# Performance work log

Hardware: AMD Instinct MI355X
Metric: run time of the kernel (lower is better)

## Reference

```python
import jax, jax.numpy as jnp
import numpy as np

HEADS = 16
DIM_HEAD = 64
SCALE = DIM_HEAD ** -0.5


def setup_inputs() -> dict:
    key = jax.random.key(0)
    k1, k2, k3, k4 = jax.random.split(key, 4)
    b, n, dim = 2, 2048, 1024
    inner = HEADS * DIM_HEAD  # 1024
    x = jax.random.normal(k1, (b, n, dim), dtype=jnp.float32)
    # binary keep-mask (multiplicative, as in the original module)
    seq_mask = (jax.random.uniform(k2, (b, n)) < 0.9).astype(jnp.float32)
    # weights stored [in, out] (transpose of torch Linear layout)
    w_qkv = jax.random.normal(k3, (dim, inner * 3), dtype=jnp.float32) * (dim ** -0.5)
    w_out = jax.random.normal(k4, (inner, dim), dtype=jnp.float32) * (inner ** -0.5)
    return {"x": x, "seq_mask": seq_mask, "w_qkv": w_qkv, "w_out": w_out}


def reference(x, seq_mask, w_qkv, w_out):
    b, n, dim = x.shape
    qkv = x @ w_qkv                                   # [b, n, 3*inner]
    q, k, v = jnp.split(qkv, 3, axis=-1)
    split_heads = lambda t: t.reshape(b, n, HEADS, DIM_HEAD).transpose(0, 2, 1, 3)
    q, k, v = split_heads(q), split_heads(k), split_heads(v)  # [b, h, n, d]
    dots = jnp.einsum('bhid,bhjd->bhij', q, k) * SCALE        # [b, h, n, n]
    # multiplicative mask, broadcast over heads and query index i; mask depends on key index j
    dots = dots * seq_mask[:, None, None, :]
    attn = jax.nn.softmax(dots, axis=-1)
    out = jnp.einsum('bhij,bhjd->bhid', attn, v)              # [b, h, n, d]
    out = out.transpose(0, 2, 1, 3).reshape(b, n, HEADS * DIM_HEAD)
    return out @ w_out                                        # dropout p=0 -> identity
```

## Files before the change

### kernel.cpp

```cpp
#include <hip/hip_runtime.h>
#include <hip/hip_bf16.h>

using bf16 = __hip_bfloat16;
typedef __attribute__((ext_vector_type(8))) short short8;
typedef __attribute__((ext_vector_type(4))) float floatx4;
typedef __attribute__((ext_vector_type(16))) float floatx16;
typedef __attribute__((ext_vector_type(4))) int int4v;

#define MFMA_BF16(a, b, c) __builtin_amdgcn_mfma_f32_16x16x32_bf16((a), (b), (c), 0, 0, 0)
#define MFMA32(a, b, c) __builtin_amdgcn_mfma_f32_32x32x16_bf16((a), (b), (c), 0, 0, 0)

#if defined(__has_builtin)
#if __has_builtin(__builtin_amdgcn_permlane32_swap)
#define HAS_PLSWAP 1
#endif
#endif

__device__ __forceinline__ void gload_lds16(const bf16* g, bf16* l) {
  __builtin_amdgcn_global_load_lds((__attribute__((address_space(1))) void*)g,
                                   (__attribute__((address_space(3))) void*)l,
                                   16, 0, 0);
}

__device__ __forceinline__ unsigned short bfbits(float f) {
  bf16 b = __float2bfloat16(f);
  return *reinterpret_cast<unsigned short*>(&b);
}

__device__ __forceinline__ unsigned pk2(float a, float b) {
  return (unsigned)bfbits(a) | ((unsigned)bfbits(b) << 16);
}

__device__ __forceinline__ int swz32(int r) { return (r & 7) ^ ((r >> 3) & 3); }

#define KSCALE 0.18033688011112042f

__global__ __launch_bounds__(256)
void probemask_k(const void* __restrict__ msrc, bf16* __restrict__ dst,
                 int* __restrict__ flag) {
  __shared__ int any;
  const int tid = threadIdx.x;
  if (tid == 0) any = 0;
  __syncthreads();
  const unsigned* mw = (const unsigned*)msrc;
  int bad = 0;
#pragma unroll
  for (int i = 0; i < 4; i++) {
    unsigned w = mw[tid * 4 + i];
    if (w != 0u && w != 0x3F800000u) bad = 1;
  }
  if (bad) atomicOr(&any, 1);
  __syncthreads();
  const int isbf = any;
  if (tid == 0) flag[0] = isbf;
  if (isbf) {
#pragma unroll
    for (int i = 0; i < 2; i++)
      ((int4*)dst)[tid * 2 + i] = ((const int4*)msrc)[tid * 2 + i];
  } else {
#pragma unroll
    for (int i = 0; i < 4; i++) {
      float4 v = ((const float4*)msrc)[tid * 4 + i];
      int o = tid * 16 + i * 4;
      dst[o + 0] = __float2bfloat16(v.x);
      dst[o + 1] = __float2bfloat16(v.y);
      dst[o + 2] = __float2bfloat16(v.z);
      dst[o + 3] = __float2bfloat16(v.w);
    }
  }
}

__global__ __launch_bounds__(256)
void cvt_k(const void* __restrict__ src, bf16* __restrict__ dst, int n,
           const int* __restrict__ flag) {
  if (*flag) return;
  int i = (blockIdx.x * 256 + threadIdx.x) * 4;
  if (i >= n) return;
  float4 v = ((const float4*)src)[i >> 2];
  dst[i + 0] = __float2bfloat16(v.x);
  dst[i + 1] = __float2bfloat16(v.y);
  dst[i + 2] = __float2bfloat16(v.z);
  dst[i + 3] = __float2bfloat16(v.w);
}

__global__ __launch_bounds__(256)
void transpose2_k(const void* __restrict__ in0, bf16* __restrict__ out0,
                  const void* __restrict__ in1, bf16* __restrict__ out1,
                  const int* __restrict__ flag) {
  __shared__ bf16 tile[32][33];
  const int isbf = *flag;
  constexpr int R = 1024;
  const void* in;
  bf16* out;
  int C, bx;
  if (blockIdx.x < 96) { in = in0; out = out0; C = 3072; bx = blockIdx.x * 32; }
  else                 { in = in1; out = out1; C = 1024; bx = (blockIdx.x - 96) * 32; }
  int by = blockIdx.y * 32;
  int tx = threadIdx.x & 31, ty = threadIdx.x >> 5;
#pragma unroll
  for (int i = 0; i < 4; i++) {
    size_t idx = (size_t)(by + ty + i * 8) * C + bx + tx;
    tile[ty + i * 8][tx] =
        isbf ? ((const bf16*)in)[idx] : __float2bfloat16(((const float*)in)[idx]);
  }
  __syncthreads();
#pragma unroll
  for (int i = 0; i < 4; i++)
    out[(size_t)(bx + ty + i * 8) * R + by + tx] = tile[tx][ty + i * 8];
}

template <int MODE>
__global__ __launch_bounds__(256, 2)
void gemm_k(const bf16* __restrict__ A, const bf16* __restrict__ Aalt,
            const bf16* __restrict__ Bt,
            bf16* __restrict__ Qo, bf16* __restrict__ Ko, bf16* __restrict__ Vo,
            void* __restrict__ Co, const bf16* __restrict__ Mk,
            const int* __restrict__ flag) {
  constexpr int K = 1024;
  __shared__ __align__(16) bf16 As[128 * 32];
  __shared__ __align__(16) bf16 Bs[128 * 32];

  const int tid = threadIdx.x;
  const int lane = tid & 63;
  const int wv = tid >> 6;
  const int wm = wv & 1, wn = wv >> 1;
  const int l15 = lane & 15, quad = lane >> 4;

  const int bm = blockIdx.y * 128;
  const int bn = blockIdx.x * 128;

  const int sml = tid >> 2;
  const int sg = (tid & 3) ^ ((sml >> 1) & 3);

  const int isbf = *flag;
  const bf16* Ab = (MODE == 0 && isbf) ? Aalt : A;

  floatx4 acc[4][4] = {};

  for (int k0 = 0; k0 < K; k0 += 32) {
    __syncthreads();
    const bf16* a0 = Ab + (size_t)(bm + sml) * K + k0 + sg * 8;
    gload_lds16(a0, &As[tid * 8]);
    gload_lds16(a0 + (size_t)64 * K, &As[2048 + tid * 8]);
    const bf16* b0 = Bt + (size_t)(bn + sml) * K + k0 + sg * 8;
    gload_lds16(b0, &Bs[tid * 8]);
    gload_lds16(b0 + (size_t)64 * K, &Bs[2048 + tid * 8]);
    __syncthreads();

    short8 af[4], bfr[4];
#pragma unroll
    for (int mi = 0; mi < 4; mi++) {
      int m = wm * 64 + mi * 16 + l15;
      af[mi] = *(const short8*)&As[m * 32 + ((quad ^ ((m >> 1) & 3)) * 8)];
    }
#pragma unroll
    for (int ni = 0; ni < 4; ni++) {
      int n = wn * 64 + ni * 16 + l15;
      bfr[ni] = *(const short8*)&Bs[n * 32 + ((quad ^ ((n >> 1) & 3)) * 8)];
    }
#pragma unroll
    for (int mi = 0; mi < 4; mi++)
#pragma unroll
      for (int ni = 0; ni < 4; ni++)
        acc[mi][ni] = MFMA_BF16(af[mi], bfr[ni], acc[mi][ni]);
  }

#pragma unroll
  for (int mi = 0; mi < 4; mi++) {
    const int row0 = bm + wm * 64 + mi * 16 + quad * 4;
#pragma unroll
    for (int ni = 0; ni < 4; ni++) {
      const int col = bn + wn * 64 + ni * 16 + l15;
      if (MODE == 0) {
        const int sec = col >> 10;
        const int cc = col & 1023;
        const int h = cc >> 6, d = cc & 63;
        const int b_idx = row0 >> 11;
        const int nn0 = row0 & 2047;
        if (sec == 0) {
          bf16* dst = Qo + (size_t)(b_idx * 16 + h) * 131072 + (size_t)nn0 * 64 + d;
#pragma unroll
          for (int r = 0; r < 4; r++) dst[r * 64] = __float2bfloat16(acc[mi][ni][r]);
        } else if (sec == 1) {
          const bf16* mrow = Mk + (size_t)b_idx * 2048 + nn0;
          bf16* dst = Ko + (size_t)(b_idx * 16 + h) * 131072 + (size_t)nn0 * 64 + d;
#pragma unroll
          for (int r = 0; r < 4; r++)
            dst[r * 64] = __float2bfloat16(acc[mi][ni][r] * KSCALE *
                                           __bfloat162float(mrow[r]));
        } else {
          bf16* dst = Vo + (size_t)(b_idx * 16 + h) * 131072 + (size_t)d * 2048 + nn0;
#pragma unroll
          for (int r = 0; r < 4; r++) dst[r] = __float2bfloat16(acc[mi][ni][r]);
        }
      } else {
        if (isbf) {
          bf16* C2 = (bf16*)Co;
#pragma unroll
          for (int r = 0; r < 4; r++)
            C2[(size_t)(row0 + r) * 1024 + col] = __float2bfloat16(acc[mi][ni][r]);
        } else {
          float* C2 = (float*)Co;
#pragma unroll
          for (int r = 0; r < 4; r++)
            C2[(size_t)(row0 + r) * 1024 + col] = acc[mi][ni][r];
        }
      }
    }
  }
}

__global__ __launch_bounds__(256, 4)
void flash_k(const bf16* __restrict__ Q, const bf16* __restrict__ K,
             const bf16* __restrict__ VT, bf16* __restrict__ AO) {
  __shared__ __align__(16) bf16 Ks[2][4096];
  __shared__ __align__(16) bf16 Vs[2][4096];
#ifndef HAS_PLSWAP
  __shared__ __align__(16) bf16 Ps[8192];
#endif

  const int tid = threadIdx.x;
  const int lane = tid & 63;
  const int w = tid >> 6;
  const int l31 = lane & 31;
  const int l5h = lane >> 5;
  const int sw = swz32(l31);

  const int qt = blockIdx.x & 15;
  const int hl = blockIdx.x >> 4;
  const int b_idx = hl >> 4, h = hl & 15;

  const bf16* Qh = Q + (size_t)hl * 131072;
  const bf16* Kh = K + (size_t)hl * 131072;
  const bf16* Vh = VT + (size_t)hl * 131072;

  const int qbase = qt * 128 + w * 32;
  const int qrow = qbase + l31;

  short8 qf[4];
#pragma unroll
  for (int c = 0; c < 4; c++)
    qf[c] = *(const short8*)&Qh[(size_t)qrow * 64 + c * 16 + l5h * 8];

  floatx16 o_acc[2] = {};
  float rsum = 0.f;

#ifndef HAS_PLSWAP
  bf16* Psw = Ps + w * 2048;
#endif

  const int sjj = tid >> 3;
  const int sgp = (tid & 7) ^ swz32(sjj);

  gload_lds16(&Kh[(size_t)sjj * 64 + sgp * 8], &Ks[0][tid * 8]);
  gload_lds16(&Kh[(size_t)(32 + sjj) * 64 + sgp * 8], &Ks[0][2048 + tid * 8]);
  gload_lds16(&Vh[(size_t)sjj * 2048 + sgp * 8], &Vs[0][tid * 8]);
  gload_lds16(&Vh[(size_t)(32 + sjj) * 2048 + sgp * 8], &Vs[0][2048 + tid * 8]);

  for (int it = 0; it < 32; ++it) {
    const int b = it & 1;
    __syncthreads();
    if (it < 31) {
      const int j1 = (it + 1) * 64;
      gload_lds16(&Kh[(size_t)(j1 + sjj) * 64 + sgp * 8], &Ks[b ^ 1][tid * 8]);
      gload_lds16(&Kh[(size_t)(j1 + 32 + sjj) * 64 + sgp * 8], &Ks[b ^ 1][2048 + tid * 8]);
      gload_lds16(&Vh[(size_t)sjj * 2048 + j1 + sgp * 8], &Vs[b ^ 1][tid * 8]);
      gload_lds16(&Vh[(size_t)(32 + sjj) * 2048 + j1 + sgp * 8], &Vs[b ^ 1][2048 + tid * 8]);
    }

    floatx16 s[2] = {};
#pragma unroll
    for (int kt = 0; kt < 2; kt++) {
      const int key = kt * 32 + l31;
#pragma unroll
      for (int c = 0; c < 4; c++) {
        const int g = c * 2 + l5h;
        short8 kf = *(const short8*)&Ks[b][key * 64 + ((g ^ sw) * 8)];
        s[kt] = MFMA32(kf, qf[c], s[kt]);
      }
    }

    float rs = 0.f;
#pragma unroll
    for (int kt = 0; kt < 2; kt++)
#pragma unroll
      for (int r = 0; r < 16; r++) {
        const float p = __builtin_amdgcn_exp2f(s[kt][r]);
        s[kt][r] = p;
        rs += p;
      }
    rs += __shfl_xor(rs, 32, 64);
    rsum += rs;

    short8 pf[4];
#ifdef HAS_PLSWAP
#pragma unroll
    for (int kt = 0; kt < 2; kt++) {
      unsigned pd[4][2];
#pragma unroll
      for (int rg = 0; rg < 4; rg++) {
        pd[rg][0] = pk2(s[kt][rg * 4 + 0], s[kt][rg * 4 + 1]);
        pd[rg][1] = pk2(s[kt][rg * 4 + 2], s[kt][rg * 4 + 3]);
      }
#pragma unroll
      for (int cp = 0; cp < 2; cp++) {
        auto ra = __builtin_amdgcn_permlane32_swap(pd[cp * 2][0], pd[cp * 2 + 1][0],
                                                   false, false);
        auto rb = __builtin_amdgcn_permlane32_swap(pd[cp * 2][1], pd[cp * 2 + 1][1],
                                                   false, false);
        int4v pi;
        pi[0] = (int)ra[0];
        pi[1] = (int)rb[0];
        pi[2] = (int)ra[1];
        pi[3] = (int)rb[1];
        pf[kt * 2 + cp] = *(short8*)&pi;
      }
    }
#else
#pragma unroll
    for (int kt = 0; kt < 2; kt++)
#pragma unroll
      for (int rg = 0; rg < 4; rg++) {
        ushort4 u;
        u.x = bfbits(s[kt][rg * 4 + 0]);
        u.y = bfbits(s[kt][rg * 4 + 1]);
        u.z = bfbits(s[kt][rg * 4 + 2]);
        u.w = bfbits(s[kt][rg * 4 + 3]);
        const int g = kt * 4 + rg;
        *(ushort4*)&Psw[l31 * 64 + ((g ^ sw) * 8) + l5h * 4] = u;
      }
    __builtin_amdgcn_wave_barrier();
#pragma unroll
    for (int c = 0; c < 4; c++) {
      const int g = c * 2 + l5h;
      pf[c] = *(const short8*)&Psw[l31 * 64 + ((g ^ sw) * 8)];
    }
#endif

#pragma unroll
    for (int dt = 0; dt < 2; dt++) {
      const int d = dt * 32 + l31;
#pragma unroll
      for (int c = 0; c < 4; c++) {
        const int g = c * 2 + l5h;
        short8 vf = *(const short8*)&Vs[b][d * 64 + ((g ^ sw) * 8)];
        o_acc[dt] = MFMA32(vf, pf[c], o_acc[dt]);
      }
    }
  }

  const float rinv = 1.f / rsum;
  bf16* orow = AO + (size_t)(b_idx * 2048 + qbase + l31) * 1024 + h * 64;
#pragma unroll
  for (int dt = 0; dt < 2; dt++)
#pragma unroll
    for (int rg = 0; rg < 4; rg++) {
      ushort4 u;
      u.x = bfbits(o_acc[dt][rg * 4 + 0] * rinv);
      u.y = bfbits(o_acc[dt][rg * 4 + 1] * rinv);
      u.z = bfbits(o_acc[dt][rg * 4 + 2] * rinv);
      u.w = bfbits(o_acc[dt][rg * 4 + 3] * rinv);
      *(ushort4*)&orow[dt * 32 + rg * 8 + l5h * 4] = u;
    }
}

extern "C" void kernel_launch(void* const* d_in, const int* in_sizes, int n_in,
                              void* d_out, int out_size, void* d_ws, size_t ws_size,
                              hipStream_t stream) {
  const void* x     = d_in[0];
  const void* mask  = d_in[1];
  const void* w_qkv = d_in[2];
  const void* w_out = d_in[3];

  bf16* ws    = (bf16*)d_ws;
  bf16* xb    = ws;
  bf16* AO    = ws;
  bf16* wqkvT = ws + 4194304;
  bf16* woutT = wqkvT + 3145728;
  bf16* Qb    = woutT + 1048576;
  bf16* Kb    = Qb + 4194304;
  bf16* maskb = Kb + 4194304;
  int*  flag  = (int*)(maskb + 4096);
  bf16* VT    = (bf16*)d_out;

  probemask_k<<<1, 256, 0, stream>>>(mask, maskb, flag);
  cvt_k<<<4096, 256, 0, stream>>>(x, xb, 4194304, flag);
  transpose2_k<<<dim3(128, 32), 256, 0, stream>>>(w_qkv, wqkvT, w_out, woutT, flag);
  gemm_k<0><<<dim3(24, 32), 256, 0, stream>>>(xb, (const bf16*)x, wqkvT, Qb, Kb, VT,
                                              nullptr, maskb, flag);
  flash_k<<<512, 256, 0, stream>>>(Qb, Kb, VT, AO);
  gemm_k<1><<<dim3(8, 32), 256, 0, stream>>>(AO, nullptr, woutT, nullptr, nullptr,
                                             nullptr, d_out, nullptr, flag);
}
```

Measured before the change: 203.9 us.

## Split flash attention key range across two wave groups per block

The flash kernel now launches 512 threads per block. Two groups of four waves each process half of the key sequence for the same 128 queries, using separate double-buffered K/V LDS regions. Their partial outputs and row sums are combined through shared memory at the end. This raises the number of waves working on each query tile, with 512 blocks on a GPU of this size, at the cost of more LDS per block, an extra reduction step and fewer blocks resident per CU.

```diff
diff --git a/kernel.cpp b/kernel.cpp
--- a/kernel.cpp
+++ b/kernel.cpp
@@ -29,6 +29,20 @@
 
 __device__ __forceinline__ unsigned pk2(float a, float b) {
   return (unsigned)bfbits(a) | ((unsigned)bfbits(b) << 16);
+}
+
+__device__ __forceinline__ void plswap(unsigned A, unsigned B, int l5h,
+                                       unsigned& out0, unsigned& out1) {
+#ifdef HAS_PLSWAP
+  auto r = __builtin_amdgcn_permlane32_swap(A, B, false, false);
+  out0 = r[0];
+  out1 = r[1];
+#else
+  unsigned sa = (unsigned)__shfl_xor((int)A, 32, 64);
+  unsigned sb = (unsigned)__shfl_xor((int)B, 32, 64);
+  out0 = l5h ? sb : A;
+  out1 = l5h ? B : sa;
+#endif
 }
 
 __device__ __forceinline__ int swz32(int r) { return (r & 7) ^ ((r >> 3) & 3); }
@@ -210,18 +224,16 @@
   }
 }
 
-__global__ __launch_bounds__(256, 4)
+__global__ __launch_bounds__(512, 2)
 void flash_k(const bf16* __restrict__ Q, const bf16* __restrict__ K,
              const bf16* __restrict__ VT, bf16* __restrict__ AO) {
-  __shared__ __align__(16) bf16 Ks[2][4096];
-  __shared__ __align__(16) bf16 Vs[2][4096];
-#ifndef HAS_PLSWAP
-  __shared__ __align__(16) bf16 Ps[8192];
-#endif
+  __shared__ __align__(16) bf16 smem[32768];
 
   const int tid = threadIdx.x;
   const int lane = tid & 63;
   const int w = tid >> 6;
+  const int strm = w >> 2;
+  const int wl = w & 3;
   const int l31 = lane & 31;
   const int l5h = lane >> 5;
   const int sw = swz32(l31);
@@ -234,8 +246,12 @@
   const bf16* Kh = K + (size_t)hl * 131072;
   const bf16* Vh = VT + (size_t)hl * 131072;
 
-  const int qbase = qt * 128 + w * 32;
+  const int qbase = qt * 128 + wl * 32;
   const int qrow = qbase + l31;
+  const int koff = strm * 1024;
+
+  bf16* KsS = smem + strm * 8192;
+  bf16* VsS = smem + 16384 + strm * 8192;
 
   short8 qf[4];
 #pragma unroll
@@ -245,27 +261,28 @@
   floatx16 o_acc[2] = {};
   float rsum = 0.f;
 
-#ifndef HAS_PLSWAP
-  bf16* Psw = Ps + w * 2048;
-#endif
-
-  const int sjj = tid >> 3;
-  const int sgp = (tid & 7) ^ swz32(sjj);
-
-  gload_lds16(&Kh[(size_t)sjj * 64 + sgp * 8], &Ks[0][tid * 8]);
-  gload_lds16(&Kh[(size_t)(32 + sjj) * 64 + sgp * 8], &Ks[0][2048 + tid * 8]);
-  gload_lds16(&Vh[(size_t)sjj * 2048 + sgp * 8], &Vs[0][tid * 8]);
-  gload_lds16(&Vh[(size_t)(32 + sjj) * 2048 + sgp * 8], &Vs[0][2048 + tid * 8]);
-
-  for (int it = 0; it < 32; ++it) {
+  const int ts = tid & 255;
+  const int sjj = ts >> 3;
+  const int sgp = (ts & 7) ^ swz32(sjj);
+
+  gload_lds16(&Kh[(size_t)(koff + sjj) * 64 + sgp * 8], &KsS[ts * 8]);
+  gload_lds16(&Kh[(size_t)(koff + 32 + sjj) * 64 + sgp * 8], &KsS[2048 + ts * 8]);
+  gload_lds16(&Vh[(size_t)sjj * 2048 + koff + sgp * 8], &VsS[ts * 8]);
+  gload_lds16(&Vh[(size_t)(32 + sjj) * 2048 + koff + sgp * 8], &VsS[2048 + ts * 8]);
+
+  for (int it = 0; it < 16; ++it) {
     const int b = it & 1;
+    bf16* Ksb = KsS + b * 4096;
+    bf16* Vsb = VsS + b * 4096;
     __syncthreads();
-    if (it < 31) {
-      const int j1 = (it + 1) * 64;
-      gload_lds16(&Kh[(size_t)(j1 + sjj) * 64 + sgp * 8], &Ks[b ^ 1][tid * 8]);
-      gload_lds16(&Kh[(size_t)(j1 + 32 + sjj) * 64 + sgp * 8], &Ks[b ^ 1][2048 + tid * 8]);
-      gload_lds16(&Vh[(size_t)sjj * 2048 + j1 + sgp * 8], &Vs[b ^ 1][tid * 8]);
-      gload_lds16(&Vh[(size_t)(32 + sjj) * 2048 + j1 + sgp * 8], &Vs[b ^ 1][2048 + tid * 8]);
+    if (it < 15) {
+      const int j1 = koff + (it + 1) * 64;
+      bf16* Ksn = KsS + (b ^ 1) * 4096;
+      bf16* Vsn = VsS + (b ^ 1) * 4096;
+      gload_lds16(&Kh[(size_t)(j1 + sjj) * 64 + sgp * 8], &Ksn[ts * 8]);
+      gload_lds16(&Kh[(size_t)(j1 + 32 + sjj) * 64 + sgp * 8], &Ksn[2048 + ts * 8]);
+      gload_lds16(&Vh[(size_t)sjj * 2048 + j1 + sgp * 8], &Vsn[ts * 8]);
+      gload_lds16(&Vh[(size_t)(32 + sjj) * 2048 + j1 + sgp * 8], &Vsn[2048 + ts * 8]);
     }
 
     floatx16 s[2] = {};
@@ -275,7 +292,7 @@
 #pragma unroll
       for (int c = 0; c < 4; c++) {
         const int g = c * 2 + l5h;
-        short8 kf = *(const short8*)&Ks[b][key * 64 + ((g ^ sw) * 8)];
+        short8 kf = *(const short8*)&Ksb[key * 64 + ((g ^ sw) * 8)];
         s[kt] = MFMA32(kf, qf[c], s[kt]);
       }
     }
@@ -293,7 +310,6 @@
     rsum += rs;
 
     short8 pf[4];
-#ifdef HAS_PLSWAP
 #pragma unroll
     for (int kt = 0; kt < 2; kt++) {
       unsigned pd[4][2];
@@ -304,38 +320,17 @@
       }
 #pragma unroll
       for (int cp = 0; cp < 2; cp++) {
-        auto ra = __builtin_amdgcn_permlane32_swap(pd[cp * 2][0], pd[cp * 2 + 1][0],
-                                                   false, false);
-        auto rb = __builtin_amdgcn_permlane32_swap(pd[cp * 2][1], pd[cp * 2 + 1][1],
-                                                   false, false);
+        unsigned ra0, ra1, rb0, rb1;
+        plswap(pd[cp * 2][0], pd[cp * 2 + 1][0], l5h, ra0, ra1);
+        plswap(pd[cp * 2][1], pd[cp * 2 + 1][1], l5h, rb0, rb1);
         int4v pi;
-        pi[0] = (int)ra[0];
-        pi[1] = (int)rb[0];
-        pi[2] = (int)ra[1];
-        pi[3] = (int)rb[1];
+        pi[0] = (int)ra0;
+        pi[1] = (int)rb0;
+        pi[2] = (int)ra1;
+        pi[3] = (int)rb1;
         pf[kt * 2 + cp] = *(short8*)&pi;
       }
     }
-#else
-#pragma unroll
-    for (int kt = 0; kt < 2; kt++)
-#pragma unroll
-      for (int rg = 0; rg < 4; rg++) {
-        ushort4 u;
-        u.x = bfbits(s[kt][rg * 4 + 0]);
-        u.y = bfbits(s[kt][rg * 4 + 1]);
-        u.z = bfbits(s[kt][rg * 4 + 2]);
-        u.w = bfbits(s[kt][rg * 4 + 3]);
-        const int g = kt * 4 + rg;
-        *(ushort4*)&Psw[l31 * 64 + ((g ^ sw) * 8) + l5h * 4] = u;
-      }
-    __builtin_amdgcn_wave_barrier();
-#pragma unroll
-    for (int c = 0; c < 4; c++) {
-      const int g = c * 2 + l5h;
-      pf[c] = *(const short8*)&Psw[l31 * 64 + ((g ^ sw) * 8)];
-    }
-#endif
 
 #pragma unroll
     for (int dt = 0; dt < 2; dt++) {
@@ -343,25 +338,45 @@
 #pragma unroll
       for (int c = 0; c < 4; c++) {
         const int g = c * 2 + l5h;
-        short8 vf = *(const short8*)&Vs[b][d * 64 + ((g ^ sw) * 8)];
+        short8 vf = *(const short8*)&Vsb[d * 64 + ((g ^ sw) * 8)];
         o_acc[dt] = MFMA32(vf, pf[c], o_acc[dt]);
       }
     }
   }
 
-  const float rinv = 1.f / rsum;
-  bf16* orow = AO + (size_t)(b_idx * 2048 + qbase + l31) * 1024 + h * 64;
-#pragma unroll
-  for (int dt = 0; dt < 2; dt++)
-#pragma unroll
-    for (int rg = 0; rg < 4; rg++) {
-      ushort4 u;
-      u.x = bfbits(o_acc[dt][rg * 4 + 0] * rinv);
-      u.y = bfbits(o_acc[dt][rg * 4 + 1] * rinv);
-      u.z = bfbits(o_acc[dt][rg * 4 + 2] * rinv);
-      u.w = bfbits(o_acc[dt][rg * 4 + 3] * rinv);
-      *(ushort4*)&orow[dt * 32 + rg * 8 + l5h * 4] = u;
-    }
+  float* comb = (float*)smem;
+  float* crs = comb + 128 * 68;
+  const int row = wl * 32 + l31;
+  __syncthreads();
+  if (strm == 1) {
+#pragma unroll
+    for (int dt = 0; dt < 2; dt++)
+#pragma unroll
+      for (int rg = 0; rg < 4; rg++) {
+        float4 v = {o_acc[dt][rg * 4 + 0], o_acc[dt][rg * 4 + 1],
+                    o_acc[dt][rg * 4 + 2], o_acc[dt][rg * 4 + 3]};
+        *(float4*)&comb[row * 68 + dt * 32 + rg * 8 + l5h * 4] = v;
+      }
+    if (l5h == 0) crs[row] = rsum;
+  }
+  __syncthreads();
+  if (strm == 0) {
+    const float rtot = rsum + crs[row];
+    const float rinv = 1.f / rtot;
+    bf16* orow = AO + (size_t)(b_idx * 2048 + qbase + l31) * 1024 + h * 64;
+#pragma unroll
+    for (int dt = 0; dt < 2; dt++)
+#pragma unroll
+      for (int rg = 0; rg < 4; rg++) {
+        float4 p = *(const float4*)&comb[row * 68 + dt * 32 + rg * 8 + l5h * 4];
+        ushort4 u;
+        u.x = bfbits((o_acc[dt][rg * 4 + 0] + p.x) * rinv);
+        u.y = bfbits((o_acc[dt][rg * 4 + 1] + p.y) * rinv);
+        u.z = bfbits((o_acc[dt][rg * 4 + 2] + p.z) * rinv);
+        u.w = bfbits((o_acc[dt][rg * 4 + 3] + p.w) * rinv);
+        *(ushort4*)&orow[dt * 32 + rg * 8 + l5h * 4] = u;
+      }
+  }
 }
 
 extern "C" void kernel_launch(void* const* d_in, const int* in_sizes, int n_in,
@@ -388,7 +403,7 @@
   transpose2_k<<<dim3(128, 32), 256, 0, stream>>>(w_qkv, wqkvT, w_out, woutT, flag);
   gemm_k<0><<<dim3(24, 32), 256, 0, stream>>>(xb, (const bf16*)x, wqkvT, Qb, Kb, VT,
                                               nullptr, maskb, flag);
-  flash_k<<<512, 256, 0, stream>>>(Qb, Kb, VT, AO);
+  flash_k<<<512, 512, 0, stream>>>(Qb, Kb, VT, AO);
   gemm_k<1><<<dim3(8, 32), 256, 0, stream>>>(AO, nullptr, woutT, nullptr, nullptr,
                                              nullptr, d_out, nullptr, flag);
 }
```

Result: faster. 194.6 us (-4.6%).
